# Kernel optimization log

Hardware: AMD Instinct MI355X
Metric: run time of the kernel (lower is better)

## Reference

```python
import jax, jax.numpy as jnp
import numpy as np

NEG_SLOPE = 0.2  # PyG GATConv default leaky_relu slope
EPS = 1e-16


def setup_inputs() -> dict:
    key = jax.random.key(0)
    ks = jax.random.split(key, 8)
    N, E, F = 50000, 1600000, 128
    L, H, C = 3, 4, 32  # layers, heads, per-head channels; H*C == F
    Dh = 32             # MLP hidden (== hidden_channels)
    x = jax.random.normal(ks[0], (N, F), jnp.float32)
    edge_index = jax.random.randint(ks[1], (2, E), 0, N, jnp.int32)
    W = jax.random.normal(ks[2], (L, F, H * C), jnp.float32) * 0.1
    att_src = jax.random.normal(ks[3], (L, H, C), jnp.float32) * 0.1
    att_dst = jax.random.normal(ks[4], (L, H, C), jnp.float32) * 0.1
    b_conv = jnp.zeros((L, H * C), jnp.float32)
    W1 = jax.random.normal(ks[5], (F + H * C, Dh), jnp.float32) * 0.1
    b1 = jnp.zeros((Dh,), jnp.float32)
    W2 = jax.random.normal(ks[6], (Dh, 1), jnp.float32) * 0.1
    b2 = jnp.zeros((1,), jnp.float32)
    return {"x": x, "edge_index": edge_index, "W": W, "att_src": att_src,
            "att_dst": att_dst, "b_conv": b_conv, "W1": W1, "b1": b1,
            "W2": W2, "b2": b2}


def _gat_layer(x, src, dst, W, a_s, a_d, b, N):
    H, C = a_s.shape
    h = (x @ W).reshape(N, H, C)                      # [N,H,C]
    alpha_s = jnp.sum(h * a_s, axis=-1)               # [N,H]
    alpha_d = jnp.sum(h * a_d, axis=-1)               # [N,H]
    e = jax.nn.leaky_relu(alpha_s[src] + alpha_d[dst], NEG_SLOPE)  # [E,H]
    # segment softmax over incoming edges of each dst node
    m = jax.ops.segment_max(e, dst, num_segments=N)
    ex = jnp.exp(e - m[dst])
    s = jax.ops.segment_sum(ex, dst, num_segments=N)
    a = ex / (s[dst] + EPS)                           # [E,H]
    out = jax.ops.segment_sum(h[src] * a[:, :, None], dst, num_segments=N)
    return out.reshape(N, H * C) + b


def reference(x, edge_index, W, att_src, att_dst, b_conv, W1, b1, W2, b2):
    N = x.shape[0]
    loops = jnp.arange(N, dtype=edge_index.dtype)
    src = jnp.concatenate([edge_index[0], loops])  # PyG GATConv adds self loops
    dst = jnp.concatenate([edge_index[1], loops])
    x0 = x
    for l in range(W.shape[0]):
        x = _gat_layer(x, src, dst, W[l], att_src[l], att_dst[l], b_conv[l], N)
    h = jnp.concatenate([x, x0], axis=-1)
    h = jax.nn.relu(h @ W1 + b1)
    return jax.nn.sigmoid(h @ W2 + b2)
```

## Files before the change

kernel.cpp:

```cpp
#include <hip/hip_runtime.h>

#define NEG_SLOPE 0.2f
#define EPSF 1e-16f
#define SEG_SHIFT 13

typedef unsigned int uint;
typedef unsigned short ushort;
typedef __attribute__((ext_vector_type(8))) short short8;
typedef __attribute__((ext_vector_type(4))) float floatx4;
typedef __attribute__((ext_vector_type(4))) uint uintx4;

static __device__ __forceinline__ ushort f2bf(float f) {
    uint u = __float_as_uint(f);
    return (ushort)((u + 0x7FFFu + ((u >> 16) & 1u)) >> 16);
}
static __device__ __forceinline__ uint pack2(float a, float b) {
    return (uint)f2bf(a) | ((uint)f2bf(b) << 16);
}
static __device__ __forceinline__ float bf_lo(uint p) { return __uint_as_float(p << 16); }
static __device__ __forceinline__ float bf_hi(uint p) { return __uint_as_float(p & 0xFFFF0000u); }
static __device__ __forceinline__ short8 u2s8(uint4 v) {
    union { uint4 u; short8 s; } c; c.u = v; return c.s;
}
static __device__ __forceinline__ void load_lds16(const void* g, void* l) {
    __builtin_amdgcn_global_load_lds(
        (const __attribute__((address_space(1))) void*)g,
        (__attribute__((address_space(3))) void*)l, 16, 0, 0);
}

#define GA_LDS_BYTES (2048 * 16 + 16 * 65 * 16)

static __device__ __forceinline__ void gemm_body(
    char* smraw, const uint4* __restrict__ xb, const uint4* __restrict__ Wp,
    const float* __restrict__ att_s, const float* __restrict__ att_d,
    uint* __restrict__ h2, float* __restrict__ alpha_s,
    float* __restrict__ alpha_d, int N, int rowBase)
{
    uint4* sW = (uint4*)smraw;
    uint4* sX = sW + 2048;
    uint* stg = (uint*)sX;

    const int t = threadIdx.x;
    const int wb = t & ~63;

#pragma unroll
    for (int i = 0; i < 8; ++i)
        load_lds16(Wp + i * 256 + t, sW + i * 256 + wb);

#pragma unroll
    for (int i = 0; i < 4; ++i) {
        int f = t + i * 256;
        int row = f >> 4, c8 = f & 15;
        uint4 v = make_uint4(0u, 0u, 0u, 0u);
        if (rowBase + row < N) v = xb[(size_t)(rowBase + row) * 16 + c8];
        sX[c8 * 65 + row] = v;
    }
    __syncthreads();

    const int w = t >> 6, lane = t & 63, q = lane >> 4, l15 = lane & 15;
    short8 xf[4];
#pragma unroll
    for (int s = 0; s < 4; ++s)
        xf[s] = u2s8(sX[(4 * s + q) * 65 + 16 * w + l15]);

    floatx4 acc[8];
#pragma unroll
    for (int ct = 0; ct < 8; ++ct) acc[ct] = (floatx4){0.f, 0.f, 0.f, 0.f};
#pragma unroll
    for (int ct = 0; ct < 8; ++ct) {
#pragma unroll
        for (int s = 0; s < 4; ++s) {
            short8 wf = u2s8(sW[(4 * s + q) * 128 + 16 * ct + l15]);
            acc[ct] = __builtin_amdgcn_mfma_f32_16x16x32_bf16(wf, xf[s], acc[ct], 0, 0, 0);
        }
    }
    __syncthreads();

    {
        const int nl = 16 * w + l15;
#pragma unroll
        for (int ct = 0; ct < 8; ++ct) {
            uint2 o;
            o.x = pack2(acc[ct][0], acc[ct][1]);
            o.y = pack2(acc[ct][2], acc[ct][3]);
            *(uint2*)(stg + nl * 65 + 8 * ct + 2 * q) = o;
        }
    }
    __syncthreads();

#pragma unroll
    for (int i = 0; i < 4; ++i) {
        int f = t + i * 256;
        int nl = f >> 4, c8 = f & 15;
        if (rowBase + nl < N)
            ((uint4*)(h2 + (size_t)(rowBase + nl) * 64))[c8] =
                *(const uint4*)(stg + nl * 65 + 4 * c8);
    }

    float ps[4], pd[4];
#pragma unroll
    for (int hd = 0; hd < 4; ++hd) {
        const float4 as0 = *(const float4*)(att_s + 32 * hd + 4 * q);
        const float4 as1 = *(const float4*)(att_s + 32 * hd + 16 + 4 * q);
        const float4 ad0 = *(const float4*)(att_d + 32 * hd + 4 * q);
        const float4 ad1 = *(const float4*)(att_d + 32 * hd + 16 + 4 * q);
        floatx4 c0 = acc[2 * hd], c1 = acc[2 * hd + 1];
        ps[hd] = c0[0] * as0.x + c0[1] * as0.y + c0[2] * as0.z + c0[3] * as0.w
               + c1[0] * as1.x + c1[1] * as1.y + c1[2] * as1.z + c1[3] * as1.w;
        pd[hd] = c0[0] * ad0.x + c0[1] * ad0.y + c0[2] * ad0.z + c0[3] * ad0.w
               + c1[0] * ad1.x + c1[1] * ad1.y + c1[2] * ad1.z + c1[3] * ad1.w;
    }
#pragma unroll
    for (int hd = 0; hd < 4; ++hd) {
        ps[hd] += __shfl_xor(ps[hd], 16);
        ps[hd] += __shfl_xor(ps[hd], 32);
        pd[hd] += __shfl_xor(pd[hd], 16);
        pd[hd] += __shfl_xor(pd[hd], 32);
    }
    const int node = rowBase + 16 * w + l15;
    if (node < N) {
        alpha_s[(size_t)node * 4 + q] = ps[q];
        alpha_d[(size_t)node * 4 + q] = pd[q];
    }
}

__global__ __launch_bounds__(256) void prep_count_kernel(
    const float* __restrict__ W, const float* __restrict__ W1,
    const float* __restrict__ x, uint4* __restrict__ Wp,
    uint4* __restrict__ W1p, uint4* __restrict__ xb,
    const int* __restrict__ ei, int E, int NB,
    int* __restrict__ bucket_count, int L, int N, int nbPrep)
{
    __shared__ int cnt[256];
    if ((int)blockIdx.x >= nbPrep) {
        cnt[threadIdx.x] = 0;
        __syncthreads();
        const int base = (blockIdx.x - nbPrep) * 2048 + threadIdx.x;
#pragma unroll
        for (int j = 0; j < 8; ++j) {
            int idx = base + j * 256;
            if (idx < E) atomicAdd(&cnt[ei[E + idx] >> 8], 1);
        }
        __syncthreads();
        int c = cnt[threadIdx.x];
        if ((int)threadIdx.x < NB && c) atomicAdd(&bucket_count[threadIdx.x], c);
        return;
    }
    int id = blockIdx.x * 256 + threadIdx.x;
    const int nW = L * 2048;
    const int nX = N * 16;
    if (id < nW) {
        int l = id >> 11, s = id & 2047;
        int chunk = s >> 7, col = s & 127;
        const float* wp = W + (size_t)l * 16384 + (chunk * 8) * 128 + col;
        uint4 pk;
        pk.x = pack2(wp[0],   wp[128]);
        pk.y = pack2(wp[256], wp[384]);
        pk.z = pack2(wp[512], wp[640]);
        pk.w = pack2(wp[768], wp[896]);
        Wp[id] = pk;
    } else if (id < nW + 1024) {
        int s = id - nW;
        int chunk = s >> 5, col = s & 31;
        const float* wp = W1 + (chunk * 8) * 32 + col;
        uint4 pk;
        pk.x = pack2(wp[0],   wp[32]);
        pk.y = pack2(wp[64],  wp[96]);
        pk.z = pack2(wp[128], wp[160]);
        pk.w = pack2(wp[192], wp[224]);
        W1p[s] = pk;
    } else if (id < nW + 1024 + nX) {
        int xid = id - nW - 1024;
        int row = xid >> 4, c8 = xid & 15;
        const float4* xp = (const float4*)(x + (size_t)row * 128 + c8 * 8);
        float4 v0 = xp[0], v1 = xp[1];
        uint4 pk;
        pk.x = pack2(v0.x, v0.y); pk.y = pack2(v0.z, v0.w);
        pk.z = pack2(v1.x, v1.y); pk.w = pack2(v1.z, v1.w);
        xb[xid] = pk;
    }
}

__global__ __launch_bounds__(256) void dist_kernel(
    const int* __restrict__ ei, int E, int NB,
    const int* __restrict__ bucket_count, int* __restrict__ bucket_cursor,
    uint* __restrict__ bdata)
{
    __shared__ int cnt[256];
    __shared__ int sc[256];
    __shared__ int bb[256];
    const int t = threadIdx.x;
    cnt[t] = 0;
    __syncthreads();
    const int base = blockIdx.x * 2048 + t;
    int srcs[8], dsts[8], rank[8];
#pragma unroll
    for (int j = 0; j < 8; ++j) {
        int idx = base + j * 256;
        if (idx < E) {
            srcs[j] = ei[idx];
            dsts[j] = ei[E + idx];
            rank[j] = atomicAdd(&cnt[dsts[j] >> 8], 1);
        } else dsts[j] = -1;
    }
    __syncthreads();
    int bc = (t < NB) ? bucket_count[t] : 0;
    sc[t] = bc;
    __syncthreads();
    for (int off = 1; off < 256; off <<= 1) {
        int x = sc[t];
        int a = (t >= off) ? sc[t - off] : 0;
        __syncthreads();
        sc[t] = x + a;
        __syncthreads();
    }
    int gbase = sc[t] - bc;
    int c = cnt[t];
    bb[t] = (t < NB && c) ? (gbase + atomicAdd(&bucket_cursor[t], c)) : 0;
    __syncthreads();
#pragma unroll
    for (int j = 0; j < 8; ++j) {
        if (dsts[j] >= 0) {
            int b = dsts[j] >> 8;
            bdata[bb[b] + rank[j]] = (uint)srcs[j] | ((uint)(dsts[j] & 255) << 16);
        }
    }
}

#define BCAP 12800
__global__ __launch_bounds__(256) void csr_gemm_kernel(
    const uint* __restrict__ bdata, const int* __restrict__ bucket_count,
    int NB, int E, int* __restrict__ row_start, ushort* __restrict__ csr_src,
    const uint4* __restrict__ xb, const uint4* __restrict__ Wp,
    const float* __restrict__ att_s, const float* __restrict__ att_d,
    uint* __restrict__ h2, float* __restrict__ alpha_s,
    float* __restrict__ alpha_d, int N)
{
    __shared__ __align__(16) char smraw[GA_LDS_BYTES];
    const int t = threadIdx.x;
    if ((int)blockIdx.x >= NB) {
        gemm_body(smraw, xb, Wp, att_s, att_d, h2, alpha_s, alpha_d, N,
                  (blockIdx.x - NB) * 64);
        return;
    }
    int* hist = (int*)smraw;
    int* cur  = hist + 2048;
    int* scn  = cur + 2048;
    int* sb   = scn + 256;
    ushort* buf = (ushort*)(sb + 256);
    const int b = blockIdx.x;

    int bc = (t < NB) ? bucket_count[t] : 0;
    sb[t] = bc;
    __syncthreads();
    for (int off = 1; off < 256; off <<= 1) {
        int x = sb[t];
        int a = (t >= off) ? sb[t - off] : 0;
        __syncthreads();
        sb[t] = x + a;
        __syncthreads();
    }
    const int beg = (b > 0) ? sb[b - 1] : 0;
    const int sz = sb[b] - beg;
    if (b == 0 && t == 0) row_start[N] = E;

#pragma unroll
    for (int j = 0; j < 8; ++j) hist[t * 8 + j] = 0;
    __syncthreads();
    for (int i = t; i < sz; i += 256) {
        uint d = bdata[beg + i];
        int key = (int)((d >> 16) << 3) | (int)((d & 0xFFFFu) >> SEG_SHIFT);
        atomicAdd(&hist[key], 1);
    }
    __syncthreads();
    int local[8]; int s = 0;
#pragma unroll
    for (int j = 0; j < 8; ++j) { local[j] = hist[t * 8 + j]; s += local[j]; }
    scn[t] = s;
    __syncthreads();
    for (int off = 1; off < 256; off <<= 1) {
        int x = scn[t];
        int a = (t >= off) ? scn[t - off] : 0;
        __syncthreads();
        scn[t] = x + a;
        __syncthreads();
    }
    int run = scn[t] - s;
#pragma unroll
    for (int j = 0; j < 8; ++j) { cur[t * 8 + j] = run; run += local[j]; }
    __syncthreads();
    int node = b * 256 + t;
    if (node < N) row_start[node] = beg + cur[t << 3];
    __syncthreads();
    if (sz <= BCAP) {
        for (int i = t; i < sz; i += 256) {
            uint d = bdata[beg + i];
            int key = (int)((d >> 16) << 3) | (int)((d & 0xFFFFu) >> SEG_SHIFT);
            int pos = atomicAdd(&cur[key], 1);
            buf[pos] = (ushort)(d & 0xFFFFu);
        }
        __syncthreads();
        for (int i = t; i < sz; i += 256)
            __builtin_nontemporal_store(buf[i], &csr_src[beg + i]);
    } else {
        for (int i = t; i < sz; i += 256) {
            uint d = bdata[beg + i];
            int key = (int)((d >> 16) << 3) | (int)((d & 0xFFFFu) >> SEG_SHIFT);
            int pos = atomicAdd(&cur[key], 1);
            csr_src[beg + pos] = (ushort)(d & 0xFFFFu);
        }
    }
}

static __device__ __forceinline__ void agg_core(
    const ushort* __restrict__ csr_src, const int* __restrict__ row_start,
    const float* __restrict__ alpha_s, const float* __restrict__ alpha_d,
    const uint* __restrict__ h2, int g, int l, int head,
    float& a0, float& a1, float& a2, float& a3,
    float& a4, float& a5, float& a6, float& a7, float& sx)
{
    const char* hbase = (const char*)h2 + (size_t)l * 16;
    const float ad = alpha_d[g * 4 + head];

    float e = alpha_s[g * 4 + head] + ad;
    e = e > 0.f ? e : NEG_SLOPE * e;
    float ex = __expf(e);
    uint4 q = *(const uint4*)(hbase + (uint)g * 256u);
    a0 = ex * bf_lo(q.x); a1 = ex * bf_hi(q.x);
    a2 = ex * bf_lo(q.y); a3 = ex * bf_hi(q.y);
    a4 = ex * bf_lo(q.z); a5 = ex * bf_hi(q.z);
    a6 = ex * bf_lo(q.w); a7 = ex * bf_hi(q.w);
    sx = ex;

    const int beg = row_start[g];
    const int end = row_start[g + 1];
    int k = beg;
    for (; k + 4 <= end; k += 4) {
        uint s0 = csr_src[k], s1 = csr_src[k + 1];
        uint s2 = csr_src[k + 2], s3 = csr_src[k + 3];
        uint4 q0 = *(const uint4*)(hbase + s0 * 256u);
        uint4 q1 = *(const uint4*)(hbase + s1 * 256u);
        uint4 q2 = *(const uint4*)(hbase + s2 * 256u);
        uint4 q3 = *(const uint4*)(hbase + s3 * 256u);
        float e0 = alpha_s[s0 * 4 + head] + ad;
        float e1 = alpha_s[s1 * 4 + head] + ad;
        float e2 = alpha_s[s2 * 4 + head] + ad;
        float e3 = alpha_s[s3 * 4 + head] + ad;
        e0 = e0 > 0.f ? e0 : NEG_SLOPE * e0;
        e1 = e1 > 0.f ? e1 : NEG_SLOPE * e1;
        e2 = e2 > 0.f ? e2 : NEG_SLOPE * e2;
        e3 = e3 > 0.f ? e3 : NEG_SLOPE * e3;
        float x0 = __expf(e0), x1 = __expf(e1);
        float x2 = __expf(e2), x3 = __expf(e3);
        a0 += x0 * bf_lo(q0.x) + x1 * bf_lo(q1.x) + x2 * bf_lo(q2.x) + x3 * bf_lo(q3.x);
        a1 += x0 * bf_hi(q0.x) + x1 * bf_hi(q1.x) + x2 * bf_hi(q2.x) + x3 * bf_hi(q3.x);
        a2 += x0 * bf_lo(q0.y) + x1 * bf_lo(q1.y) + x2 * bf_lo(q2.y) + x3 * bf_lo(q3.y);
        a3 += x0 * bf_hi(q0.y) + x1 * bf_hi(q1.y) + x2 * bf_hi(q2.y) + x3 * bf_hi(q3.y);
        a4 += x0 * bf_lo(q0.z) + x1 * bf_lo(q1.z) + x2 * bf_lo(q2.z) + x3 * bf_lo(q3.z);
        a5 += x0 * bf_hi(q0.z) + x1 * bf_hi(q1.z) + x2 * bf_hi(q2.z) + x3 * bf_hi(q3.z);
        a6 += x0 * bf_lo(q0.w) + x1 * bf_lo(q1.w) + x2 * bf_lo(q2.w) + x3 * bf_lo(q3.w);
        a7 += x0 * bf_hi(q0.w) + x1 * bf_hi(q1.w) + x2 * bf_hi(q2.w) + x3 * bf_hi(q3.w);
        sx += x0 + x1 + x2 + x3;
    }
    for (; k < end; ++k) {
        uint s0 = csr_src[k];
        float e0 = alpha_s[s0 * 4 + head] + ad;
        uint4 q0 = *(const uint4*)(hbase + s0 * 256u);
        e0 = e0 > 0.f ? e0 : NEG_SLOPE * e0;
        float x0 = __expf(e0);
        a0 += x0 * bf_lo(q0.x); a1 += x0 * bf_hi(q0.x);
        a2 += x0 * bf_lo(q0.y); a3 += x0 * bf_hi(q0.y);
        a4 += x0 * bf_lo(q0.z); a5 += x0 * bf_hi(q0.z);
        a6 += x0 * bf_lo(q0.w); a7 += x0 * bf_hi(q0.w);
        sx += x0;
    }
}

__global__ __launch_bounds__(256) void aggemm_kernel(
    const ushort* __restrict__ csr_src, const int* __restrict__ row_start,
    const float* __restrict__ alpha_s, const float* __restrict__ alpha_d,
    const uint* __restrict__ h2in, const float* __restrict__ b,
    const uint4* __restrict__ Wnext,
    const float* __restrict__ att_s, const float* __restrict__ att_d,
    uint* __restrict__ h2out, float* __restrict__ alpha_s_out,
    float* __restrict__ alpha_d_out, int N)
{
    __shared__ __align__(16) uint4 tile[16 * 17];
    const int t = threadIdx.x;
    const int nodeBase = blockIdx.x * 16;
    const int gl = t >> 4;
    const int g = nodeBase + gl;
    const int l = t & 15;
    const bool active = g < N;

    uint4 o = make_uint4(0u, 0u, 0u, 0u);
    if (active) {
        float a0, a1, a2, a3, a4, a5, a6, a7, sx;
        agg_core(csr_src, row_start, alpha_s, alpha_d, h2in, g, l, l >> 2,
                 a0, a1, a2, a3, a4, a5, a6, a7, sx);
        const float inv = 1.f / (sx + EPSF);
        const float4 b0 = ((const float4*)b)[l * 2];
        const float4 b1 = ((const float4*)b)[l * 2 + 1];
        o.x = pack2(b0.x + a0 * inv, b0.y + a1 * inv);
        o.y = pack2(b0.z + a2 * inv, b0.w + a3 * inv);
        o.z = pack2(b1.x + a4 * inv, b1.y + a5 * inv);
        o.w = pack2(b1.z + a6 * inv, b1.w + a7 * inv);
    }
    tile[gl * 17 + l] = o;
    __syncthreads();

    const int w = t >> 6, lane = t & 63, q = lane >> 4, l15 = lane & 15;
    floatx4 acc0 = (floatx4){0.f, 0.f, 0.f, 0.f};
    floatx4 acc1 = (floatx4){0.f, 0.f, 0.f, 0.f};
#pragma unroll
    for (int s = 0; s < 4; ++s) {
        short8 xfr = u2s8(tile[l15 * 17 + 4 * s + q]);
        short8 wf0 = u2s8(Wnext[(4 * s + q) * 128 + 16 * (2 * w) + l15]);
        short8 wf1 = u2s8(Wnext[(4 * s + q) * 128 + 16 * (2 * w + 1) + l15]);
        acc0 = __builtin_amdgcn_mfma_f32_16x16x32_bf16(wf0, xfr, acc0, 0, 0, 0);
        acc1 = __builtin_amdgcn_mfma_f32_16x16x32_bf16(wf1, xfr, acc1, 0, 0, 0);
    }
    __syncthreads();

    uint* stg = (uint*)tile;
    {
        uint2 o0, o1;
        o0.x = pack2(acc0[0], acc0[1]); o0.y = pack2(acc0[2], acc0[3]);
        o1.x = pack2(acc1[0], acc1[1]); o1.y = pack2(acc1[2], acc1[3]);
        *(uint2*)(stg + l15 * 65 + 16 * w + 2 * q) = o0;
        *(uint2*)(stg + l15 * 65 + 16 * w + 8 + 2 * q) = o1;
    }
    __syncthreads();
    {
        int nl = t >> 4, c8 = t & 15;
        if (nodeBase + nl < N)
            ((uint4*)(h2out + (size_t)(nodeBase + nl) * 64))[c8] =
                *(const uint4*)(stg + nl * 65 + 4 * c8);
    }

    const float4 as0 = *(const float4*)(att_s + 32 * w + 4 * q);
    const float4 as1 = *(const float4*)(att_s + 32 * w + 16 + 4 * q);
    const float4 ad0 = *(const float4*)(att_d + 32 * w + 4 * q);
    const float4 ad1 = *(const float4*)(att_d + 32 * w + 16 + 4 * q);
    float ps = acc0[0] * as0.x + acc0[1] * as0.y + acc0[2] * as0.z + acc0[3] * as0.w
             + acc1[0] * as1.x + acc1[1] * as1.y + acc1[2] * as1.z + acc1[3] * as1.w;
    float pd = acc0[0] * ad0.x + acc0[1] * ad0.y + acc0[2] * ad0.z + acc0[3] * ad0.w
             + acc1[0] * ad1.x + acc1[1] * ad1.y + acc1[2] * ad1.z + acc1[3] * ad1.w;
    ps += __shfl_xor(ps, 16); ps += __shfl_xor(ps, 32);
    pd += __shfl_xor(pd, 16); pd += __shfl_xor(pd, 32);
    const int node = nodeBase + l15;
    if (node < N && q == 0) {
        alpha_s_out[(size_t)node * 4 + w] = ps;
        alpha_d_out[(size_t)node * 4 + w] = pd;
    }
}

__global__ __launch_bounds__(256) void aggmlp_kernel(
    const ushort* __restrict__ csr_src, const int* __restrict__ row_start,
    const float* __restrict__ alpha_s, const float* __restrict__ alpha_d,
    const uint* __restrict__ h2in, const float* __restrict__ b,
    const uint4* __restrict__ xb0, const uint4* __restrict__ W1p,
    const float* __restrict__ b1, const float* __restrict__ W2,
    const float* __restrict__ b2, float* __restrict__ out, int N)
{
    __shared__ __align__(16) uint4 tile[16 * 33];
    __shared__ float pr[32];
    const int t = threadIdx.x;
    const int nodeBase = blockIdx.x * 16;
    const int gl = t >> 4;
    const int g = nodeBase + gl;
    const int l = t & 15;

    {
        uintx4 v = (uintx4){0u, 0u, 0u, 0u};
        if (g < N)
            v = __builtin_nontemporal_load(
                (const uintx4*)(xb0 + (size_t)g * 16 + l));
        union { uintx4 x; uint4 u; } cc; cc.x = v;
        tile[gl * 33 + 16 + l] = cc.u;
    }

    uint4 o = make_uint4(0u, 0u, 0u, 0u);
    if (g < N) {
        float a0, a1, a2, a3, a4, a5, a6, a7, sx;
        agg_core(csr_src, row_start, alpha_s, alpha_d, h2in, g, l, l >> 2,
                 a0, a1, a2, a3, a4, a5, a6, a7, sx);
        const float inv = 1.f / (sx + EPSF);
        const float4 b0 = ((const float4*)b)[l * 2];
        const float4 b1v = ((const float4*)b)[l * 2 + 1];
        o.x = pack2(b0.x + a0 * inv, b0.y + a1 * inv);
        o.y = pack2(b0.z + a2 * inv, b0.w + a3 * inv);
        o.z = pack2(b1v.x + a4 * inv, b1v.y + a5 * inv);
        o.w = pack2(b1v.z + a6 * inv, b1v.w + a7 * inv);
    }
    tile[gl * 33 + l] = o;
    __syncthreads();

    const int w = t >> 6, lane = t & 63, q = lane >> 4, l15 = lane & 15;
    if (w < 2) {
        floatx4 acc = (floatx4){0.f, 0.f, 0.f, 0.f};
#pragma unroll
        for (int s = 0; s < 8; ++s) {
            short8 a = u2s8(tile[l15 * 33 + 4 * s + q]);
            short8 bb = u2s8(W1p[(4 * s + q) * 32 + 16 * w + l15]);
            acc = __builtin_amdgcn_mfma_f32_16x16x32_bf16(a, bb, acc, 0, 0, 0);
        }
        const int col = 16 * w + l15;
        const float b1c = b1[col], w2c = W2[col];
#pragma unroll
        for (int r = 0; r < 4; ++r) {
            float v = acc[r] + b1c;
            v = v > 0.f ? v : 0.f;
            float p = v * w2c;
            p += __shfl_xor(p, 1);
            p += __shfl_xor(p, 2);
            p += __shfl_xor(p, 4);
            p += __shfl_xor(p, 8);
            if (l15 == 0) pr[w * 16 + 4 * q + r] = p;
        }
    }
    __syncthreads();
    if (t < 16) {
        int node = nodeBase + t;
        if (node < N) {
            float z = pr[t] + pr[16 + t] + b2[0];
            out[node] = 1.f / (1.f + __expf(-z));
        }
    }
}

extern "C" void kernel_launch(void* const* d_in, const int* in_sizes, int n_in,
                              void* d_out, int out_size, void* d_ws, size_t ws_size,
                              hipStream_t stream)
{
    const float* x       = (const float*)d_in[0];
    const int*   ei      = (const int*)d_in[1];
    const float* W       = (const float*)d_in[2];
    const float* att_src = (const float*)d_in[3];
    const float* att_dst = (const float*)d_in[4];
    const float* b_conv  = (const float*)d_in[5];
    const float* W1      = (const float*)d_in[6];
    const float* b1      = (const float*)d_in[7];
    const float* W2      = (const float*)d_in[8];
    const float* b2      = (const float*)d_in[9];
    float* outp = (float*)d_out;

    const int N = in_sizes[0] / 128;
    const int E = in_sizes[1] / 2;
    const int L = in_sizes[2] / (128 * 128);
    const int NB = (N + 255) >> 8;

    char* ws = (char*)d_ws;
    uint*  h2a      = (uint*)ws;
    uint*  h2b      = h2a + (size_t)N * 64;
    uint4* xb0      = (uint4*)(h2b + (size_t)N * 64);
    float* alphaA_s = (float*)(xb0 + (size_t)N * 16);
    float* alphaA_d = alphaA_s + (size_t)N * 4;
    float* alphaB_s = alphaA_d + (size_t)N * 4;
    float* alphaB_d = alphaB_s + (size_t)N * 4;
    uint4* Wp       = (uint4*)(alphaB_d + (size_t)N * 4);
    uint4* W1p      = Wp + (size_t)L * 2048;
    int* bucket_count  = (int*)(W1p + 1024);
    int* bucket_cursor = bucket_count + 256;
    int* row_start     = bucket_cursor + 256;
    uint* bdata        = (uint*)(row_start + N + 1);
    ushort* csr_src    = (ushort*)(bdata + E);

    const int nbE = (E + 2047) / 2048;
    const int gBlocks = (N + 63) / 64;
    const int aggBlocks = (N + 15) / 16;
    const int prepItems = L * 2048 + 1024 + N * 16;
    const int nbPrep = (prepItems + 255) / 256;

    (void)hipMemsetAsync(bucket_count, 0, 512 * sizeof(int), stream);

    prep_count_kernel<<<nbPrep + nbE, 256, 0, stream>>>(
        W, W1, x, Wp, W1p, xb0, ei, E, NB, bucket_count, L, N, nbPrep);

    dist_kernel<<<nbE, 256, 0, stream>>>(ei, E, NB, bucket_count,
                                         bucket_cursor, bdata);

    csr_gemm_kernel<<<NB + gBlocks, 256, 0, stream>>>(
        bdata, bucket_count, NB, E, row_start, csr_src,
        xb0, Wp, att_src, att_dst, h2a, alphaA_s, alphaA_d, N);

    aggemm_kernel<<<aggBlocks, 256, 0, stream>>>(
        csr_src, row_start, alphaA_s, alphaA_d, h2a,
        b_conv + 0 * 128, Wp + (size_t)1 * 2048,
        att_src + (size_t)1 * 128, att_dst + (size_t)1 * 128,
        h2b, alphaB_s, alphaB_d, N);

    aggemm_kernel<<<aggBlocks, 256, 0, stream>>>(
        csr_src, row_start, alphaB_s, alphaB_d, h2b,
        b_conv + (size_t)1 * 128, Wp + (size_t)2 * 2048,
        att_src + (size_t)2 * 128, att_dst + (size_t)2 * 128,
        h2a, alphaA_s, alphaA_d, N);

    aggmlp_kernel<<<aggBlocks, 256, 0, stream>>>(
        csr_src, row_start, alphaA_s, alphaA_d, h2a,
        b_conv + (size_t)2 * 128, xb0, W1p, b1, W2, b2, outp, N);
}
```

Baseline: 315.8 us.

## Sort nodes by in-degree so aggregation blocks process similar-degree nodes

Adds a degree histogram in the CSR build kernel and a new perm kernel that counting-sorts nodes by in-degree, capped at 511. The aggregation kernels then map each 16-node block to permuted node ids, so the 16-thread groups in a block have similar loop lengths. This targets load imbalance and divergence between the node groups that share a block. It costs an extra kernel launch, a larger memset and indirect, scattered writes of outputs.

```diff
diff --git a/kernel.cpp b/kernel.cpp
--- a/kernel.cpp
+++ b/kernel.cpp
@@ -231,6 +231,7 @@
 __global__ __launch_bounds__(256) void csr_gemm_kernel(
     const uint* __restrict__ bdata, const int* __restrict__ bucket_count,
     int NB, int E, int* __restrict__ row_start, ushort* __restrict__ csr_src,
+    int* __restrict__ deg_hist,
     const uint4* __restrict__ xb, const uint4* __restrict__ Wp,
     const float* __restrict__ att_s, const float* __restrict__ att_d,
     uint* __restrict__ h2, float* __restrict__ alpha_s,
@@ -310,6 +311,63 @@
             csr_src[beg + pos] = (ushort)(d & 0xFFFFu);
         }
     }
+    __syncthreads();
+    hist[t] = 0; hist[t + 256] = 0;
+    __syncthreads();
+    if (node < N) atomicAdd(&hist[s < 511 ? s : 511], 1);
+    __syncthreads();
+    if (hist[t]) atomicAdd(&deg_hist[t], hist[t]);
+    if (hist[t + 256]) atomicAdd(&deg_hist[t + 256], hist[t + 256]);
+}
+
+__global__ __launch_bounds__(256) void perm_kernel(
+    const int* __restrict__ row_start, const int* __restrict__ deg_hist,
+    int* __restrict__ gcur, int* __restrict__ perm, int N)
+{
+    __shared__ int base[512];
+    __shared__ int ps[256];
+    __shared__ int cnt[512];
+    __shared__ int bbase[512];
+    const int t = threadIdx.x;
+    int b0 = deg_hist[2 * t], b1 = deg_hist[2 * t + 1];
+    ps[t] = b0 + b1;
+    __syncthreads();
+    for (int off = 1; off < 256; off <<= 1) {
+        int x = ps[t];
+        int a = (t >= off) ? ps[t - off] : 0;
+        __syncthreads();
+        ps[t] = x + a;
+        __syncthreads();
+    }
+    int ex = ps[t] - (b0 + b1);
+    base[2 * t] = ex;
+    base[2 * t + 1] = ex + b0;
+    cnt[t] = 0; cnt[t + 256] = 0;
+    __syncthreads();
+    const int nbase = blockIdx.x * 2048 + t;
+    int dg[8], rk[8];
+#pragma unroll
+    for (int j = 0; j < 8; ++j) {
+        int g = nbase + j * 256;
+        if (g < N) {
+            int d = row_start[g + 1] - row_start[g];
+            if (d > 511) d = 511;
+            dg[j] = d;
+            rk[j] = atomicAdd(&cnt[d], 1);
+        } else dg[j] = -1;
+    }
+    __syncthreads();
+    {
+        int c = cnt[t];
+        bbase[t] = c ? atomicAdd(&gcur[t], c) : 0;
+        c = cnt[t + 256];
+        bbase[t + 256] = c ? atomicAdd(&gcur[t + 256], c) : 0;
+    }
+    __syncthreads();
+#pragma unroll
+    for (int j = 0; j < 8; ++j)
+        if (dg[j] >= 0)
+            perm[base[dg[j]] + bbase[dg[j]] + rk[j]] = nbase + j * 256;
 }
 
 static __device__ __forceinline__ void agg_core(
@@ -378,6 +436,7 @@
 
 __global__ __launch_bounds__(256) void aggemm_kernel(
     const ushort* __restrict__ csr_src, const int* __restrict__ row_start,
+    const int* __restrict__ perm,
     const float* __restrict__ alpha_s, const float* __restrict__ alpha_d,
     const uint* __restrict__ h2in, const float* __restrict__ b,
     const uint4* __restrict__ Wnext,
@@ -386,15 +445,17 @@
     float* __restrict__ alpha_d_out, int N)
 {
     __shared__ __align__(16) uint4 tile[16 * 17];
+    __shared__ int sperm[16];
     const int t = threadIdx.x;
     const int nodeBase = blockIdx.x * 16;
     const int gl = t >> 4;
-    const int g = nodeBase + gl;
     const int l = t & 15;
-    const bool active = g < N;
+    if (t < 16) sperm[t] = (nodeBase + t < N) ? perm[nodeBase + t] : -1;
+    __syncthreads();
+    const int g = sperm[gl];
 
     uint4 o = make_uint4(0u, 0u, 0u, 0u);
-    if (active) {
+    if (g >= 0) {
         float a0, a1, a2, a3, a4, a5, a6, a7, sx;
         agg_core(csr_src, row_start, alpha_s, alpha_d, h2in, g, l, l >> 2,
                  a0, a1, a2, a3, a4, a5, a6, a7, sx);
@@ -433,8 +494,9 @@
     __syncthreads();
     {
         int nl = t >> 4, c8 = t & 15;
-        if (nodeBase + nl < N)
-            ((uint4*)(h2out + (size_t)(nodeBase + nl) * 64))[c8] =
+        int node = sperm[nl];
+        if (node >= 0)
+            ((uint4*)(h2out + (size_t)node * 64))[c8] =
                 *(const uint4*)(stg + nl * 65 + 4 * c8);
     }
 
@@ -448,8 +510,8 @@
              + acc1[0] * ad1.x + acc1[1] * ad1.y + acc1[2] * ad1.z + acc1[3] * ad1.w;
     ps += __shfl_xor(ps, 16); ps += __shfl_xor(ps, 32);
     pd += __shfl_xor(pd, 16); pd += __shfl_xor(pd, 32);
-    const int node = nodeBase + l15;
-    if (node < N && q == 0) {
+    const int node = sperm[l15];
+    if (node >= 0 && q == 0) {
         alpha_s_out[(size_t)node * 4 + w] = ps;
         alpha_d_out[(size_t)node * 4 + w] = pd;
     }
@@ -457,6 +519,7 @@
 
 __global__ __launch_bounds__(256) void aggmlp_kernel(
     const ushort* __restrict__ csr_src, const int* __restrict__ row_start,
+    const int* __restrict__ perm,
     const float* __restrict__ alpha_s, const float* __restrict__ alpha_d,
     const uint* __restrict__ h2in, const float* __restrict__ b,
     const uint4* __restrict__ xb0, const uint4* __restrict__ W1p,
@@ -465,15 +528,18 @@
 {
     __shared__ __align__(16) uint4 tile[16 * 33];
     __shared__ float pr[32];
+    __shared__ int sperm[16];
     const int t = threadIdx.x;
     const int nodeBase = blockIdx.x * 16;
     const int gl = t >> 4;
-    const int g = nodeBase + gl;
     const int l = t & 15;
+    if (t < 16) sperm[t] = (nodeBase + t < N) ? perm[nodeBase + t] : -1;
+    __syncthreads();
+    const int g = sperm[gl];
 
     {
         uintx4 v = (uintx4){0u, 0u, 0u, 0u};
-        if (g < N)
+        if (g >= 0)
             v = __builtin_nontemporal_load(
                 (const uintx4*)(xb0 + (size_t)g * 16 + l));
         union { uintx4 x; uint4 u; } cc; cc.x = v;
@@ -481,7 +547,7 @@
     }
 
     uint4 o = make_uint4(0u, 0u, 0u, 0u);
-    if (g < N) {
+    if (g >= 0) {
         float a0, a1, a2, a3, a4, a5, a6, a7, sx;
         agg_core(csr_src, row_start, alpha_s, alpha_d, h2in, g, l, l >> 2,
                  a0, a1, a2, a3, a4, a5, a6, a7, sx);
@@ -521,8 +587,8 @@
     }
     __syncthreads();
     if (t < 16) {
-        int node = nodeBase + t;
-        if (node < N) {
+        int node = sperm[t];
+        if (node >= 0) {
             float z = pr[t] + pr[16 + t] + b2[0];
             out[node] = 1.f / (1.f + __expf(-z));
         }
@@ -562,17 +628,21 @@
     uint4* W1p      = Wp + (size_t)L * 2048;
     int* bucket_count  = (int*)(W1p + 1024);
     int* bucket_cursor = bucket_count + 256;
-    int* row_start     = bucket_cursor + 256;
-    uint* bdata        = (uint*)(row_start + N + 1);
+    int* deg_hist      = bucket_cursor + 256;
+    int* gcur          = deg_hist + 512;
+    int* row_start     = gcur + 512;
+    int* perm          = row_start + N + 1;
+    uint* bdata        = (uint*)(perm + N);
     ushort* csr_src    = (ushort*)(bdata + E);
 
     const int nbE = (E + 2047) / 2048;
     const int gBlocks = (N + 63) / 64;
     const int aggBlocks = (N + 15) / 16;
+    const int permBlocks = (N + 2047) / 2048;
     const int prepItems = L * 2048 + 1024 + N * 16;
     const int nbPrep = (prepItems + 255) / 256;
 
-    (void)hipMemsetAsync(bucket_count, 0, 512 * sizeof(int), stream);
+    (void)hipMemsetAsync(bucket_count, 0, 1536 * sizeof(int), stream);
 
     prep_count_kernel<<<nbPrep + nbE, 256, 0, stream>>>(
         W, W1, x, Wp, W1p, xb0, ei, E, NB, bucket_count, L, N, nbPrep);
@@ -581,22 +651,25 @@
                                          bucket_cursor, bdata);
 
     csr_gemm_kernel<<<NB + gBlocks, 256, 0, stream>>>(
-        bdata, bucket_count, NB, E, row_start, csr_src,
+        bdata, bucket_count, NB, E, row_start, csr_src, deg_hist,
         xb0, Wp, att_src, att_dst, h2a, alphaA_s, alphaA_d, N);
 
+    perm_kernel<<<permBlocks, 256, 0, stream>>>(row_start, deg_hist, gcur,
+                                                perm, N);
+
     aggemm_kernel<<<aggBlocks, 256, 0, stream>>>(
-        csr_src, row_start, alphaA_s, alphaA_d, h2a,
+        csr_src, row_start, perm, alphaA_s, alphaA_d, h2a,
         b_conv + 0 * 128, Wp + (size_t)1 * 2048,
         att_src + (size_t)1 * 128, att_dst + (size_t)1 * 128,
         h2b, alphaB_s, alphaB_d, N);
 
     aggemm_kernel<<<aggBlocks, 256, 0, stream>>>(
-        csr_src, row_start, alphaB_s, alphaB_d, h2b,
+        csr_src, row_start, perm, alphaB_s, alphaB_d, h2b,
         b_conv + (size_t)1 * 128, Wp + (size_t)2 * 2048,
         att_src + (size_t)2 * 128, att_dst + (size_t)2 * 128,
         h2a, alphaA_s, alphaA_d, N);
 
     aggmlp_kernel<<<aggBlocks, 256, 0, stream>>>(
-        csr_src, row_start, alphaA_s, alphaA_d, h2a,
+        csr_src, row_start, perm, alphaA_s, alphaA_d, h2a,
         b_conv + (size_t)2 * 128, xb0, W1p, b1, W2, b2, outp, N);
 }
```

New measurement: 342.4 us. +8.4%, slower.

## Sort nodes by in-degree within buckets to balance aggregation warps

Applied to the files above, without the earlier changes.

While building the CSR, each 256-node bucket also computes a counting-sort permutation of its nodes by clamped in-degree and writes it to a perm array. The aggregation kernels then process nodes in permuted order, so each 16-node block (and each wavefront) handles nodes of similar degree. This is meant to cut divergence and tail imbalance caused by uneven degrees inside a wavefront. It adds a per-bucket scan, one perm lookup per block, and scattered output writes instead of contiguous ones.

```diff
diff --git a/kernel.cpp b/kernel.cpp
--- a/kernel.cpp
+++ b/kernel.cpp
@@ -231,6 +231,7 @@
 __global__ __launch_bounds__(256) void csr_gemm_kernel(
     const uint* __restrict__ bdata, const int* __restrict__ bucket_count,
     int NB, int E, int* __restrict__ row_start, ushort* __restrict__ csr_src,
+    int* __restrict__ perm,
     const uint4* __restrict__ xb, const uint4* __restrict__ Wp,
     const float* __restrict__ att_s, const float* __restrict__ att_d,
     uint* __restrict__ h2, float* __restrict__ alpha_s,
@@ -310,6 +311,27 @@
             csr_src[beg + pos] = (ushort)(d & 0xFFFFu);
         }
     }
+
+    __syncthreads();
+    hist[t] = 0;
+    __syncthreads();
+    int dclamp = s < 255 ? s : 255;
+    int rbin = (node < N) ? atomicAdd(&hist[dclamp], 1) : 0;
+    __syncthreads();
+    int bc2 = hist[t];
+    scn[t] = bc2;
+    __syncthreads();
+    for (int off = 1; off < 256; off <<= 1) {
+        int x = scn[t];
+        int a = (t >= off) ? scn[t - off] : 0;
+        __syncthreads();
+        scn[t] = x + a;
+        __syncthreads();
+    }
+    cur[t] = scn[t] - bc2;
+    __syncthreads();
+    if (node < N)
+        perm[b * 256 + cur[dclamp] + rbin] = node;
 }
 
 static __device__ __forceinline__ void agg_core(
@@ -378,6 +400,7 @@
 
 __global__ __launch_bounds__(256) void aggemm_kernel(
     const ushort* __restrict__ csr_src, const int* __restrict__ row_start,
+    const int* __restrict__ perm,
     const float* __restrict__ alpha_s, const float* __restrict__ alpha_d,
     const uint* __restrict__ h2in, const float* __restrict__ b,
     const uint4* __restrict__ Wnext,
@@ -386,15 +409,17 @@
     float* __restrict__ alpha_d_out, int N)
 {
     __shared__ __align__(16) uint4 tile[16 * 17];
+    __shared__ int sperm[16];
     const int t = threadIdx.x;
     const int nodeBase = blockIdx.x * 16;
     const int gl = t >> 4;
-    const int g = nodeBase + gl;
     const int l = t & 15;
-    const bool active = g < N;
+    if (t < 16) sperm[t] = (nodeBase + t < N) ? perm[nodeBase + t] : -1;
+    __syncthreads();
+    const int g = sperm[gl];
 
     uint4 o = make_uint4(0u, 0u, 0u, 0u);
-    if (active) {
+    if (g >= 0) {
         float a0, a1, a2, a3, a4, a5, a6, a7, sx;
         agg_core(csr_src, row_start, alpha_s, alpha_d, h2in, g, l, l >> 2,
                  a0, a1, a2, a3, a4, a5, a6, a7, sx);
@@ -433,8 +458,9 @@
     __syncthreads();
     {
         int nl = t >> 4, c8 = t & 15;
-        if (nodeBase + nl < N)
-            ((uint4*)(h2out + (size_t)(nodeBase + nl) * 64))[c8] =
+        int node = sperm[nl];
+        if (node >= 0)
+            ((uint4*)(h2out + (size_t)node * 64))[c8] =
                 *(const uint4*)(stg + nl * 65 + 4 * c8);
     }
 
@@ -448,8 +474,8 @@
              + acc1[0] * ad1.x + acc1[1] * ad1.y + acc1[2] * ad1.z + acc1[3] * ad1.w;
     ps += __shfl_xor(ps, 16); ps += __shfl_xor(ps, 32);
     pd += __shfl_xor(pd, 16); pd += __shfl_xor(pd, 32);
-    const int node = nodeBase + l15;
-    if (node < N && q == 0) {
+    const int node = sperm[l15];
+    if (node >= 0 && q == 0) {
         alpha_s_out[(size_t)node * 4 + w] = ps;
         alpha_d_out[(size_t)node * 4 + w] = pd;
     }
@@ -457,6 +483,7 @@
 
 __global__ __launch_bounds__(256) void aggmlp_kernel(
     const ushort* __restrict__ csr_src, const int* __restrict__ row_start,
+    const int* __restrict__ perm,
     const float* __restrict__ alpha_s, const float* __restrict__ alpha_d,
     const uint* __restrict__ h2in, const float* __restrict__ b,
     const uint4* __restrict__ xb0, const uint4* __restrict__ W1p,
@@ -465,15 +492,18 @@
 {
     __shared__ __align__(16) uint4 tile[16 * 33];
     __shared__ float pr[32];
+    __shared__ int sperm[16];
     const int t = threadIdx.x;
     const int nodeBase = blockIdx.x * 16;
     const int gl = t >> 4;
-    const int g = nodeBase + gl;
     const int l = t & 15;
+    if (t < 16) sperm[t] = (nodeBase + t < N) ? perm[nodeBase + t] : -1;
+    __syncthreads();
+    const int g = sperm[gl];
 
     {
         uintx4 v = (uintx4){0u, 0u, 0u, 0u};
-        if (g < N)
+        if (g >= 0)
             v = __builtin_nontemporal_load(
                 (const uintx4*)(xb0 + (size_t)g * 16 + l));
         union { uintx4 x; uint4 u; } cc; cc.x = v;
@@ -481,7 +511,7 @@
     }
 
     uint4 o = make_uint4(0u, 0u, 0u, 0u);
-    if (g < N) {
+    if (g >= 0) {
         float a0, a1, a2, a3, a4, a5, a6, a7, sx;
         agg_core(csr_src, row_start, alpha_s, alpha_d, h2in, g, l, l >> 2,
                  a0, a1, a2, a3, a4, a5, a6, a7, sx);
@@ -521,8 +551,8 @@
     }
     __syncthreads();
     if (t < 16) {
-        int node = nodeBase + t;
-        if (node < N) {
+        int node = sperm[t];
+        if (node >= 0) {
             float z = pr[t] + pr[16 + t] + b2[0];
             out[node] = 1.f / (1.f + __expf(-z));
         }
@@ -563,7 +593,8 @@
     int* bucket_count  = (int*)(W1p + 1024);
     int* bucket_cursor = bucket_count + 256;
     int* row_start     = bucket_cursor + 256;
-    uint* bdata        = (uint*)(row_start + N + 1);
+    int* perm          = row_start + N + 1;
+    uint* bdata        = (uint*)(perm + N);
     ushort* csr_src    = (ushort*)(bdata + E);
 
     const int nbE = (E + 2047) / 2048;
@@ -581,22 +612,22 @@
                                          bucket_cursor, bdata);
 
     csr_gemm_kernel<<<NB + gBlocks, 256, 0, stream>>>(
-        bdata, bucket_count, NB, E, row_start, csr_src,
+        bdata, bucket_count, NB, E, row_start, csr_src, perm,
         xb0, Wp, att_src, att_dst, h2a, alphaA_s, alphaA_d, N);
 
     aggemm_kernel<<<aggBlocks, 256, 0, stream>>>(
-        csr_src, row_start, alphaA_s, alphaA_d, h2a,
+        csr_src, row_start, perm, alphaA_s, alphaA_d, h2a,
         b_conv + 0 * 128, Wp + (size_t)1 * 2048,
         att_src + (size_t)1 * 128, att_dst + (size_t)1 * 128,
         h2b, alphaB_s, alphaB_d, N);
 
     aggemm_kernel<<<aggBlocks, 256, 0, stream>>>(
-        csr_src, row_start, alphaB_s, alphaB_d, h2b,
+        csr_src, row_start, perm, alphaB_s, alphaB_d, h2b,
         b_conv + (size_t)1 * 128, Wp + (size_t)2 * 2048,
         att_src + (size_t)2 * 128, att_dst + (size_t)2 * 128,
         h2a, alphaA_s, alphaA_d, N);
 
     aggmlp_kernel<<<aggBlocks, 256, 0, stream>>>(
-        csr_src, row_start, alphaA_s, alphaA_d, h2a,
+        csr_src, row_start, perm, alphaA_s, alphaA_d, h2a,
         b_conv + (size_t)2 * 128, xb0, W1p, b1, W2, b2, outp, N);
 }
```

Measured after the change: 347.0 us. 1.1x slower.
